# Kernel optimization log

Hardware: AMD Instinct MI355X
Metric: run time of the kernel (lower is better)

The kernel has to match this reference:

```python
import jax, jax.numpy as jnp
import numpy as np

NUM_CLASSES = 5  # config['training']['num_classes_per_task']


def _conv(x, w, b):
    # x: [N,C,H,W], w: [O,I,kh,kw] (torch OIHW), valid padding, stride 1
    y = jax.lax.conv_general_dilated(
        x, w, window_strides=(1, 1), padding='VALID',
        dimension_numbers=('NCHW', 'OIHW', 'NCHW'))
    return y + b[None, :, None, None]


def _maxpool2(x):
    return jax.lax.reduce_window(x, -jnp.inf, jax.lax.max,
                                 (1, 1, 2, 2), (1, 1, 2, 2), 'VALID')


def _lenet(x, c1w, c1b, c2w, c2b, f1w, f1b, f2w, f2b, f3w, f3b):
    h = _maxpool2(jax.nn.relu(_conv(x, c1w, c1b)))   # [N,6,14,14]
    h = _maxpool2(jax.nn.relu(_conv(h, c2w, c2b)))   # [N,16,5,5]
    h = h.reshape(h.shape[0], -1)                     # [N,400]
    h = jax.nn.relu(h @ f1w.T + f1b)                  # [N,120]
    h = jax.nn.relu(h @ f2w.T + f2b)                  # [N,84]
    return h @ f3w.T + f3b                            # [N,64] embeddings


def setup_inputs() -> dict:
    key = jax.random.key(0)
    ks = jax.random.split(key, 7)
    def w(k, shape, fan_in):
        return jax.random.normal(k, shape, jnp.float32) * (1.0 / np.sqrt(fan_in))
    return {
        'x': jax.random.normal(ks[0], (20480, 3, 32, 32), jnp.float32),
        'c1w': w(ks[1], (6, 3, 5, 5), 3 * 25), 'c1b': jnp.zeros((6,), jnp.float32),
        'c2w': w(ks[2], (16, 6, 5, 5), 6 * 25), 'c2b': jnp.zeros((16,), jnp.float32),
        'f1w': w(ks[3], (120, 400), 400), 'f1b': jnp.zeros((120,), jnp.float32),
        'f2w': w(ks[4], (84, 120), 120), 'f2b': jnp.zeros((84,), jnp.float32),
        'f3w': w(ks[5], (64, 84), 84), 'f3b': jnp.zeros((64,), jnp.float32),
    }


def reference(x, c1w, c1b, c2w, c2b, f1w, f1b, f2w, f2b, f3w, f3b):
    emb = _lenet(x, c1w, c1b, c2w, c2b, f1w, f1b, f2w, f2b, f3w, f3b)  # [N,64]
    # prototypes = embeddings.sum() / num_classes  (scalar, as in source)
    proto = emb.sum() / NUM_CLASSES
    result = jax.nn.softmax(emb, axis=1)
    # sqrt((result - proto)^2) elementwise == |result - proto|; the python
    # per-sample list-comprehension just rebuilds this same [N,64] tensor.
    return jnp.sqrt(jnp.square(result - proto))
```

## Files before the change

### kernel.cpp

```cpp
#include <hip/hip_runtime.h>
#include <math.h>

typedef __attribute__((ext_vector_type(8))) short short8;
typedef __attribute__((ext_vector_type(4))) float f32x4;
typedef __attribute__((ext_vector_type(4))) unsigned short us4v;

__device__ __forceinline__ unsigned short f2bf(float f) {
    unsigned u = __float_as_uint(f);
    return (unsigned short)((u + 0x7FFFu + ((u >> 16) & 1u)) >> 16);
}
__device__ __forceinline__ unsigned cvtpk(float lo, float hi) {
    unsigned r;
    asm("v_cvt_pk_bf16_f32 %0, %1, %2" : "=v"(r) : "v"(lo), "v"(hi));
    return r;
}
__device__ __forceinline__ unsigned short f2bf1(float v) {
    return (unsigned short)(cvtpk(v, 0.f) & 0xffffu);
}
__device__ __forceinline__ float fmax_x8(float v) {
    int s = __builtin_amdgcn_mov_dpp(__float_as_int(v), 0x128, 0xf, 0xf, true);
    return fmaxf(v, __int_as_float(s));
}

#define C1T_SS 3464
#define C1_RS 36
#define P1R 1176
#define P2S 424
#define A1S 136
#define A2S 104

__global__ __launch_bounds__(256, 3) void conv12fc_mfma(
    const float* __restrict__ x,
    const unsigned short* __restrict__ c1wf, const float* __restrict__ c1b,
    const unsigned short* __restrict__ c2wf, const float* __restrict__ c2b,
    const unsigned short* __restrict__ wb1, const float* __restrict__ f1b,
    const unsigned short* __restrict__ wb2, const float* __restrict__ f2b,
    const unsigned short* __restrict__ wb3, const float* __restrict__ f3b,
    float* __restrict__ emb, float* __restrict__ part)
{
    __shared__ __align__(16) unsigned short img[2 * C1T_SS];
    __shared__ __align__(16) unsigned short p1s[16 * P1R + 16];
    __shared__ float rsum[4];
    const int t = threadIdx.x;
    const int lane = t & 63, w = t >> 6;
    const int grp = lane >> 4, c = lane & 15;
    const int smp = c >> 3, q = c & 7;

    if (t < 192) {
        int s = t / 96, rr = t - s * 96;
        *(uint2*)&img[s * C1T_SS + rr * C1_RS + 32] = make_uint2(0u, 0u);
    }
    if (t < 2) {
        *(uint4*)&img[t * C1T_SS + 3456] = make_uint4(0u, 0u, 0u, 0u);
        *(uint4*)&p1s[16 * P1R + t * 8] = make_uint4(0u, 0u, 0u, 0u);
    }

    short8 wf1[5][4];
#pragma unroll
    for (int s = 0; s < 5; s++)
#pragma unroll
        for (int off = 0; off < 4; off++)
            wf1[s][off] = *(const short8*)&c1wf[(((s * 4 + off) * 4 + grp) * 16 + c) * 8];
    int ciA[5], kpA[5];
#pragma unroll
    for (int s = 0; s < 5; s++) {
        int b = s * 4 + grp; if (b > 17) b = 17;
        ciA[s] = b / 6; kpA[s] = b % 6;
    }
    const float bias1 = (c < 6) ? c1b[c] : 0.f;

    const float4* xs4 = (const float4*)(x + (size_t)blockIdx.x * 49152);
    float4 r[6];

#pragma unroll
    for (int k = 0; k < 6; k++) r[k] = xs4[k * 256 + t];

    for (int st = 0; st < 8; st++) {
#pragma unroll
        for (int k = 0; k < 6; k++) {
            int f = k * 256 + t;
            int s = (f >= 768) ? 1 : 0;
            int w4 = f - s * 768;
            int ci = w4 >> 8, rem = w4 & 255, y = rem >> 3, xq = rem & 7;
            uint2 pk = make_uint2(cvtpk(r[k].x, r[k].y), cvtpk(r[k].z, r[k].w));
            *(uint2*)&img[s * C1T_SS + (ci * 32 + y) * C1_RS + xq * 4] = pk;
        }
        __syncthreads();

        if (st < 7) {
#pragma unroll
            for (int k = 0; k < 6; k++) r[k] = xs4[(st + 1) * 1536 + k * 256 + t];
        }

        for (int py = w; py < 14; py += 4) {
            f32x4 a00 = {0.f,0.f,0.f,0.f}, a01 = a00, a10 = a00, a11 = a00;
#pragma unroll
            for (int s = 0; s < 5; s++) {
                int e = smp * C1T_SS + (ciA[s] * 32 + py * 2 + kpA[s]) * C1_RS + q * 4;
                union { us4v h[2]; short8 v; } af;
                af.h[0] = *(const us4v*)&img[e];
                af.h[1] = *(const us4v*)&img[e + 4];
                a00 = __builtin_amdgcn_mfma_f32_16x16x32_bf16(af.v, wf1[s][0], a00, 0, 0, 0);
                a01 = __builtin_amdgcn_mfma_f32_16x16x32_bf16(af.v, wf1[s][1], a01, 0, 0, 0);
                a10 = __builtin_amdgcn_mfma_f32_16x16x32_bf16(af.v, wf1[s][2], a10, 0, 0, 0);
                a11 = __builtin_amdgcn_mfma_f32_16x16x32_bf16(af.v, wf1[s][3], a11, 0, 0, 0);
            }
            f32x4 pe2, po2;
#pragma unroll
            for (int i = 0; i < 4; i++) {
                pe2[i] = fmax_x8(fmaxf(a00[i], a01[i]));
                po2[i] = fmax_x8(fmaxf(a10[i], a11[i]));
            }
            if (c < 6) {
#pragma unroll
                for (int i = 0; i < 4; i++) {
                    int m = grp * 4 + i;
                    int qo = m & 7;
                    if (qo < 7) {
                        int sm = m >> 3;
                        float v0 = fmaxf(pe2[i] + bias1, 0.f);
                        float v1 = fmaxf(po2[i] + bias1, 0.f);
                        *(unsigned*)&p1s[(2 * st + sm) * P1R + (c * 14 + py) * 14 + qo * 2]
                            = cvtpk(v0, v1);
                    }
                }
            }
        }
        __syncthreads();
    }

    short8 wf2[8][2];
#pragma unroll
    for (int s = 0; s < 8; s++)
#pragma unroll
        for (int off = 0; off < 2; off++)
            wf2[s][off] = *(const short8*)&c2wf[(((s * 2 + off) * 4 + grp) * 16 + c) * 8];
    int ciB[8], kyB[8];
#pragma unroll
    for (int s = 0; s < 8; s++) {
        int b = s * 4 + grp; if (b > 29) b = 29;
        ciB[s] = b / 5; kyB[s] = b % 5;
    }
    const float bias2 = c2b[c];

    unsigned pkbuf[7][2];
#pragma unroll
    for (int j = 0; j < 7; j++) {
        const int item = w + j * 4;
        if (item < 25) {
            const int py = item / 5, px = item % 5;
            f32x4 a00 = {0.f,0.f,0.f,0.f}, a01 = a00, a10 = a00, a11 = a00;
#pragma unroll
            for (int s = 0; s < 8; s++) {
                int rbase = ciB[s] * 14 + kyB[s] + py * 2;
#pragma unroll
                for (int yo = 0; yo < 2; yo++) {
                    int e = c * P1R + (rbase + yo) * 14 + px * 2;
                    union { unsigned u[4]; short8 v; } af;
                    af.u[0] = *(const unsigned*)&p1s[e];
                    af.u[1] = *(const unsigned*)&p1s[e + 2];
                    af.u[2] = *(const unsigned*)&p1s[e + 4];
                    af.u[3] = *(const unsigned*)&p1s[e + 6];
                    if (yo == 0) {
                        a00 = __builtin_amdgcn_mfma_f32_16x16x32_bf16(af.v, wf2[s][0], a00, 0, 0, 0);
                        a01 = __builtin_amdgcn_mfma_f32_16x16x32_bf16(af.v, wf2[s][1], a01, 0, 0, 0);
                    } else {
                        a10 = __builtin_amdgcn_mfma_f32_16x16x32_bf16(af.v, wf2[s][0], a10, 0, 0, 0);
                        a11 = __builtin_amdgcn_mfma_f32_16x16x32_bf16(af.v, wf2[s][1], a11, 0, 0, 0);
                    }
                }
            }
            float v0 = fmaxf(fmaxf(fmaxf(a00[0], a01[0]), fmaxf(a10[0], a11[0])) + bias2, 0.f);
            float v1 = fmaxf(fmaxf(fmaxf(a00[1], a01[1]), fmaxf(a10[1], a11[1])) + bias2, 0.f);
            float v2 = fmaxf(fmaxf(fmaxf(a00[2], a01[2]), fmaxf(a10[2], a11[2])) + bias2, 0.f);
            float v3 = fmaxf(fmaxf(fmaxf(a00[3], a01[3]), fmaxf(a10[3], a11[3])) + bias2, 0.f);
            pkbuf[j][0] = cvtpk(v0, v1);
            pkbuf[j][1] = cvtpk(v2, v3);
        }
    }
    __syncthreads();

    unsigned short* p2t = p1s;
#pragma unroll
    for (int j = 0; j < 7; j++) {
        const int item = w + j * 4;
        if (item < 25) {
#pragma unroll
            for (int i = 0; i < 4; i++) {
                unsigned v = pkbuf[j][i >> 1] >> ((i & 1) * 16);
                p2t[(grp * 4 + i) * P2S + c * 25 + item] = (unsigned short)v;
            }
        }
    }
    if (t < 32) {
        int s = t >> 1, h = t & 1;
        *(uint4*)&p2t[s * P2S + 400 + h * 8] = make_uint4(0u, 0u, 0u, 0u);
    }
    __syncthreads();

    unsigned short* a1s = img;
    unsigned short* a2s = img + 16 * A1S;
    {
        f32x4 acc[2] = {{0.f,0.f,0.f,0.f},{0.f,0.f,0.f,0.f}};
        const int sb = c * P2S;
#pragma unroll
        for (int ks = 0; ks < 13; ks++) {
            short8 a = *(const short8*)&p2t[sb + ks * 32 + grp * 8];
#pragma unroll
            for (int j = 0; j < 2; j++) {
                int o = (w + 4 * j) * 16 + c;
                short8 b = *(const short8*)&wb1[o * 416 + ks * 32 + grp * 8];
                acc[j] = __builtin_amdgcn_mfma_f32_16x16x32_bf16(a, b, acc[j], 0, 0, 0);
            }
        }
        __syncthreads();
#pragma unroll
        for (int j = 0; j < 2; j++) {
            int o = (w + 4 * j) * 16 + c;
            float bias = (o < 120) ? f1b[o] : 0.f;
#pragma unroll
            for (int i = 0; i < 4; i++)
                a1s[(grp * 4 + i) * A1S + o] = f2bf1(fmaxf(acc[j][i] + bias, 0.f));
        }
    }
    __syncthreads();

    {
        f32x4 acc[2] = {{0.f,0.f,0.f,0.f},{0.f,0.f,0.f,0.f}};
        const int sb = c * A1S;
#pragma unroll
        for (int ks = 0; ks < 4; ks++) {
            short8 a = *(const short8*)&a1s[sb + ks * 32 + grp * 8];
#pragma unroll
            for (int j = 0; j < 2; j++) {
                int nt = w + 4 * j;
                if (nt < 6) {
                    int o = nt * 16 + c;
                    short8 b = *(const short8*)&wb2[o * 128 + ks * 32 + grp * 8];
                    acc[j] = __builtin_amdgcn_mfma_f32_16x16x32_bf16(a, b, acc[j], 0, 0, 0);
                }
            }
        }
        __syncthreads();
#pragma unroll
        for (int j = 0; j < 2; j++) {
            int nt = w + 4 * j;
            if (nt < 6) {
                int o = nt * 16 + c;
                float bias = (o < 84) ? f2b[o] : 0.f;
#pragma unroll
                for (int i = 0; i < 4; i++)
                    a2s[(grp * 4 + i) * A2S + o] = f2bf1(fmaxf(acc[j][i] + bias, 0.f));
            }
        }
    }
    __syncthreads();

    {
        f32x4 acc = {0.f,0.f,0.f,0.f};
        const int sb = c * A2S;
        const int o = w * 16 + c;
#pragma unroll
        for (int ks = 0; ks < 3; ks++) {
            short8 a = *(const short8*)&a2s[sb + ks * 32 + grp * 8];
            short8 b = *(const short8*)&wb3[o * 96 + ks * 32 + grp * 8];
            acc = __builtin_amdgcn_mfma_f32_16x16x32_bf16(a, b, acc, 0, 0, 0);
        }
        const float bias = f3b[o];
        float psum = 0.f;
#pragma unroll
        for (int i = 0; i < 4; i++) {
            float v = acc[i] + bias;
            emb[((size_t)blockIdx.x * 16 + grp * 4 + i) * 64 + o] = v;
            psum += v;
        }
#pragma unroll
        for (int off = 32; off; off >>= 1) psum += __shfl_xor(psum, off);
        if (lane == 0) rsum[w] = psum;
        __syncthreads();
        if (t == 0) part[blockIdx.x] = (rsum[0] + rsum[1]) + (rsum[2] + rsum[3]);
    }
}

__global__ __launch_bounds__(256) void prep_weights(
    const float* __restrict__ c1w, const float* __restrict__ c2w,
    const float* __restrict__ f1w, const float* __restrict__ f2w,
    const float* __restrict__ f3w,
    unsigned short* __restrict__ wb1, unsigned short* __restrict__ wb2,
    unsigned short* __restrict__ wb3,
    unsigned short* __restrict__ c1wf, unsigned short* __restrict__ c2wf)
{
    const int t0 = blockIdx.x * 256 + threadIdx.x;
    const int stride = gridDim.x * 256;
    for (int i = t0; i < 128 * 416; i += stride) {
        int o = i / 416, k = i % 416;
        wb1[i] = f2bf((o < 120 && k < 400) ? f1w[o * 400 + k] : 0.f);
    }
    for (int i = t0; i < 96 * 128; i += stride) {
        int o = i / 128, k = i % 128;
        wb2[i] = f2bf((o < 84 && k < 120) ? f2w[o * 120 + k] : 0.f);
    }
    for (int i = t0; i < 64 * 96; i += stride) {
        int o = i / 96, k = i % 96;
        wb3[i] = f2bf((k < 84) ? f3w[o * 84 + k] : 0.f);
    }
    for (int i = t0; i < 10240; i += stride) {
        int j = i & 7, c = (i >> 3) & 15, grp = (i >> 7) & 3;
        int off = (i >> 9) & 3, s = i >> 11;
        int b = s * 4 + grp;
        int ci = b / 6, kp = b % 6;
        int kx = j - off;
        float v = 0.f;
        if (b < 18 && kx >= 0 && kx <= 4) {
            if (c < 6 && kp <= 4)
                v = c1w[c * 75 + ci * 25 + kp * 5 + kx];
            else if (c >= 8 && c < 14 && kp >= 1)
                v = c1w[(c - 8) * 75 + ci * 25 + (kp - 1) * 5 + kx];
        }
        c1wf[i] = f2bf(v);
    }
    for (int i = t0; i < 8192; i += stride) {
        int j = i & 7, c = (i >> 3) & 15, grp = (i >> 7) & 3;
        int off = (i >> 9) & 1, s = i >> 10;
        int b = s * 4 + grp;
        int kx = j - off;
        float v = 0.f;
        if (b < 30 && kx >= 0 && kx <= 4) {
            int ci = b / 5, ky = b % 5;
            v = c2w[c * 150 + ci * 25 + ky * 5 + kx];
        }
        c2wf[i] = f2bf(v);
    }
}

__global__ __launch_bounds__(256) void softmax_abs(float* __restrict__ io,
                                                   const float* __restrict__ part) {
    const int lane = threadIdx.x & 63;
    const int row = (blockIdx.x << 2) + (threadIdx.x >> 6);
    float e = io[(size_t)row * 64 + lane];
    float ps = 0.f;
#pragma unroll
    for (int k = 0; k < 20; k++) ps += part[k * 64 + lane];
#pragma unroll
    for (int off = 32; off; off >>= 1) ps += __shfl_xor(ps, off);
    const float proto = ps / 5.0f;
    float m = e;
#pragma unroll
    for (int off = 32; off; off >>= 1) m = fmaxf(m, __shfl_xor(m, off));
    float p = expf(e - m);
    float s = p;
#pragma unroll
    for (int off = 32; off; off >>= 1) s += __shfl_xor(s, off);
    io[(size_t)row * 64 + lane] = fabsf(p / s - proto);
}

extern "C" void kernel_launch(void* const* d_in, const int* in_sizes, int n_in,
                              void* d_out, int out_size, void* d_ws, size_t ws_size,
                              hipStream_t stream) {
    const float* x   = (const float*)d_in[0];
    const float* c1w = (const float*)d_in[1];
    const float* c1b = (const float*)d_in[2];
    const float* c2w = (const float*)d_in[3];
    const float* c2b = (const float*)d_in[4];
    const float* f1w = (const float*)d_in[5];
    const float* f1b = (const float*)d_in[6];
    const float* f2w = (const float*)d_in[7];
    const float* f2b = (const float*)d_in[8];
    const float* f3w = (const float*)d_in[9];
    const float* f3b = (const float*)d_in[10];
    float* out = (float*)d_out;

    const int N = in_sizes[0] / 3072;
    float* part = (float*)d_ws;
    unsigned short* wb1  = (unsigned short*)((char*)d_ws + 8192);
    unsigned short* wb2  = wb1 + 128 * 416;
    unsigned short* wb3  = wb2 + 96 * 128;
    unsigned short* c1wf = wb3 + 64 * 96;
    unsigned short* c2wf = c1wf + 10240;

    prep_weights<<<64, 256, 0, stream>>>(c1w, c2w, f1w, f2w, f3w,
                                         wb1, wb2, wb3, c1wf, c2wf);
    conv12fc_mfma<<<N / 16, 256, 0, stream>>>(x, c1wf, c1b, c2wf, c2b,
                                              wb1, f1b, wb2, f2b, wb3, f3b,
                                              out, part);
    softmax_abs<<<N / 4, 256, 0, stream>>>(out, part);
}
```

Before: 94.26 us.

## Halve samples per block and reuse shifted conv1 fragments to cut registers and LDS

Each block now handles 8 samples instead of 16, which halves the pooled-conv1 LDS buffer and doubles the grid. Occupancy is raised to 4 blocks per CU. Conv1 keeps only two weight fragments and builds the odd-x input fragment by shifting loaded bf16 values, so register use drops. Conv2 maps the y-offset into lanes instead of separate accumulators. The FC stages now mask off half of their MFMA rows, which wastes MFMA work, and the softmax kernel reads twice as many partial sums.

```diff
diff --git a/kernel.cpp b/kernel.cpp
--- a/kernel.cpp
+++ b/kernel.cpp
@@ -29,7 +29,7 @@
 #define A1S 136
 #define A2S 104
 
-__global__ __launch_bounds__(256, 3) void conv12fc_mfma(
+__global__ __launch_bounds__(256, 4) void conv12fc_mfma(
     const float* __restrict__ x,
     const unsigned short* __restrict__ c1wf, const float* __restrict__ c1b,
     const unsigned short* __restrict__ c2wf, const float* __restrict__ c2b,
@@ -39,7 +39,7 @@
     float* __restrict__ emb, float* __restrict__ part)
 {
     __shared__ __align__(16) unsigned short img[2 * C1T_SS];
-    __shared__ __align__(16) unsigned short p1s[16 * P1R + 16];
+    __shared__ __align__(16) unsigned short p1s[8 * P1R + 16];
     __shared__ float rsum[4];
     const int t = threadIdx.x;
     const int lane = t & 63, w = t >> 6;
@@ -52,14 +52,14 @@
     }
     if (t < 2) {
         *(uint4*)&img[t * C1T_SS + 3456] = make_uint4(0u, 0u, 0u, 0u);
-        *(uint4*)&p1s[16 * P1R + t * 8] = make_uint4(0u, 0u, 0u, 0u);
-    }
-
-    short8 wf1[5][4];
+        *(uint4*)&p1s[8 * P1R + t * 8] = make_uint4(0u, 0u, 0u, 0u);
+    }
+
+    short8 wf1[5][2];
 #pragma unroll
     for (int s = 0; s < 5; s++)
 #pragma unroll
-        for (int off = 0; off < 4; off++)
+        for (int off = 0; off < 2; off++)
             wf1[s][off] = *(const short8*)&c1wf[(((s * 4 + off) * 4 + grp) * 16 + c) * 8];
     int ciA[5], kpA[5];
 #pragma unroll
@@ -69,13 +69,13 @@
     }
     const float bias1 = (c < 6) ? c1b[c] : 0.f;
 
-    const float4* xs4 = (const float4*)(x + (size_t)blockIdx.x * 49152);
+    const float4* xs4 = (const float4*)(x + (size_t)blockIdx.x * 24576);
     float4 r[6];
 
 #pragma unroll
     for (int k = 0; k < 6; k++) r[k] = xs4[k * 256 + t];
 
-    for (int st = 0; st < 8; st++) {
+    for (int st = 0; st < 4; st++) {
 #pragma unroll
         for (int k = 0; k < 6; k++) {
             int f = k * 256 + t;
@@ -87,7 +87,7 @@
         }
         __syncthreads();
 
-        if (st < 7) {
+        if (st < 3) {
 #pragma unroll
             for (int k = 0; k < 6; k++) r[k] = xs4[(st + 1) * 1536 + k * 256 + t];
         }
@@ -97,13 +97,17 @@
 #pragma unroll
             for (int s = 0; s < 5; s++) {
                 int e = smp * C1T_SS + (ciA[s] * 32 + py * 2 + kpA[s]) * C1_RS + q * 4;
-                union { us4v h[2]; short8 v; } af;
-                af.h[0] = *(const us4v*)&img[e];
-                af.h[1] = *(const us4v*)&img[e + 4];
-                a00 = __builtin_amdgcn_mfma_f32_16x16x32_bf16(af.v, wf1[s][0], a00, 0, 0, 0);
-                a01 = __builtin_amdgcn_mfma_f32_16x16x32_bf16(af.v, wf1[s][1], a01, 0, 0, 0);
-                a10 = __builtin_amdgcn_mfma_f32_16x16x32_bf16(af.v, wf1[s][2], a10, 0, 0, 0);
-                a11 = __builtin_amdgcn_mfma_f32_16x16x32_bf16(af.v, wf1[s][3], a11, 0, 0, 0);
+                us4v h0 = *(const us4v*)&img[e];
+                us4v h1 = *(const us4v*)&img[e + 4];
+                ushort2 h2 = *(const ushort2*)&img[e + 8];
+                short8 A0 = { (short)h0[0],(short)h0[1],(short)h0[2],(short)h0[3],
+                              (short)h1[0],(short)h1[1],(short)h1[2],(short)h1[3] };
+                short8 A2 = { (short)h0[2],(short)h0[3],(short)h1[0],(short)h1[1],
+                              (short)h1[2],(short)h1[3],(short)h2.x,(short)h2.y };
+                a00 = __builtin_amdgcn_mfma_f32_16x16x32_bf16(A0, wf1[s][0], a00, 0, 0, 0);
+                a01 = __builtin_amdgcn_mfma_f32_16x16x32_bf16(A0, wf1[s][1], a01, 0, 0, 0);
+                a10 = __builtin_amdgcn_mfma_f32_16x16x32_bf16(A2, wf1[s][0], a10, 0, 0, 0);
+                a11 = __builtin_amdgcn_mfma_f32_16x16x32_bf16(A2, wf1[s][1], a11, 0, 0, 0);
             }
             f32x4 pe2, po2;
 #pragma unroll
@@ -142,40 +146,30 @@
         ciB[s] = b / 5; kyB[s] = b % 5;
     }
     const float bias2 = c2b[c];
-
-    unsigned pkbuf[7][2];
+    const int arow2 = (c >> 1) * P1R;
+    const int yoff = c & 1;
+
+    unsigned pkbuf[7];
 #pragma unroll
     for (int j = 0; j < 7; j++) {
         const int item = w + j * 4;
         if (item < 25) {
             const int py = item / 5, px = item % 5;
-            f32x4 a00 = {0.f,0.f,0.f,0.f}, a01 = a00, a10 = a00, a11 = a00;
+            f32x4 a0 = {0.f,0.f,0.f,0.f}, a1 = a0;
 #pragma unroll
             for (int s = 0; s < 8; s++) {
-                int rbase = ciB[s] * 14 + kyB[s] + py * 2;
-#pragma unroll
-                for (int yo = 0; yo < 2; yo++) {
-                    int e = c * P1R + (rbase + yo) * 14 + px * 2;
-                    union { unsigned u[4]; short8 v; } af;
-                    af.u[0] = *(const unsigned*)&p1s[e];
-                    af.u[1] = *(const unsigned*)&p1s[e + 2];
-                    af.u[2] = *(const unsigned*)&p1s[e + 4];
-                    af.u[3] = *(const unsigned*)&p1s[e + 6];
-                    if (yo == 0) {
-                        a00 = __builtin_amdgcn_mfma_f32_16x16x32_bf16(af.v, wf2[s][0], a00, 0, 0, 0);
-                        a01 = __builtin_amdgcn_mfma_f32_16x16x32_bf16(af.v, wf2[s][1], a01, 0, 0, 0);
-                    } else {
-                        a10 = __builtin_amdgcn_mfma_f32_16x16x32_bf16(af.v, wf2[s][0], a10, 0, 0, 0);
-                        a11 = __builtin_amdgcn_mfma_f32_16x16x32_bf16(af.v, wf2[s][1], a11, 0, 0, 0);
-                    }
-                }
-            }
-            float v0 = fmaxf(fmaxf(fmaxf(a00[0], a01[0]), fmaxf(a10[0], a11[0])) + bias2, 0.f);
-            float v1 = fmaxf(fmaxf(fmaxf(a00[1], a01[1]), fmaxf(a10[1], a11[1])) + bias2, 0.f);
-            float v2 = fmaxf(fmaxf(fmaxf(a00[2], a01[2]), fmaxf(a10[2], a11[2])) + bias2, 0.f);
-            float v3 = fmaxf(fmaxf(fmaxf(a00[3], a01[3]), fmaxf(a10[3], a11[3])) + bias2, 0.f);
-            pkbuf[j][0] = cvtpk(v0, v1);
-            pkbuf[j][1] = cvtpk(v2, v3);
+                int e = arow2 + (ciB[s] * 14 + py * 2 + yoff + kyB[s]) * 14 + px * 2;
+                union { unsigned u[4]; short8 v; } af;
+                af.u[0] = *(const unsigned*)&p1s[e];
+                af.u[1] = *(const unsigned*)&p1s[e + 2];
+                af.u[2] = *(const unsigned*)&p1s[e + 4];
+                af.u[3] = *(const unsigned*)&p1s[e + 6];
+                a0 = __builtin_amdgcn_mfma_f32_16x16x32_bf16(af.v, wf2[s][0], a0, 0, 0, 0);
+                a1 = __builtin_amdgcn_mfma_f32_16x16x32_bf16(af.v, wf2[s][1], a1, 0, 0, 0);
+            }
+            float v0 = fmaxf(fmaxf(fmaxf(a0[0], a0[1]), fmaxf(a1[0], a1[1])) + bias2, 0.f);
+            float v1 = fmaxf(fmaxf(fmaxf(a0[2], a0[3]), fmaxf(a1[2], a1[3])) + bias2, 0.f);
+            pkbuf[j] = cvtpk(v0, v1);
         }
     }
     __syncthreads();
@@ -185,11 +179,8 @@
     for (int j = 0; j < 7; j++) {
         const int item = w + j * 4;
         if (item < 25) {
-#pragma unroll
-            for (int i = 0; i < 4; i++) {
-                unsigned v = pkbuf[j][i >> 1] >> ((i & 1) * 16);
-                p2t[(grp * 4 + i) * P2S + c * 25 + item] = (unsigned short)v;
-            }
+            p2t[(grp * 2 + 0) * P2S + c * 25 + item] = (unsigned short)(pkbuf[j] & 0xffffu);
+            p2t[(grp * 2 + 1) * P2S + c * 25 + item] = (unsigned short)(pkbuf[j] >> 16);
         }
     }
     if (t < 32) {
@@ -219,8 +210,10 @@
             int o = (w + 4 * j) * 16 + c;
             float bias = (o < 120) ? f1b[o] : 0.f;
 #pragma unroll
-            for (int i = 0; i < 4; i++)
-                a1s[(grp * 4 + i) * A1S + o] = f2bf1(fmaxf(acc[j][i] + bias, 0.f));
+            for (int i = 0; i < 4; i++) {
+                int s = grp * 4 + i;
+                if (s < 8) a1s[s * A1S + o] = f2bf1(fmaxf(acc[j][i] + bias, 0.f));
+            }
         }
     }
     __syncthreads();
@@ -249,8 +242,10 @@
                 int o = nt * 16 + c;
                 float bias = (o < 84) ? f2b[o] : 0.f;
 #pragma unroll
-                for (int i = 0; i < 4; i++)
-                    a2s[(grp * 4 + i) * A2S + o] = f2bf1(fmaxf(acc[j][i] + bias, 0.f));
+                for (int i = 0; i < 4; i++) {
+                    int s = grp * 4 + i;
+                    if (s < 8) a2s[s * A2S + o] = f2bf1(fmaxf(acc[j][i] + bias, 0.f));
+                }
             }
         }
     }
@@ -270,9 +265,12 @@
         float psum = 0.f;
 #pragma unroll
         for (int i = 0; i < 4; i++) {
-            float v = acc[i] + bias;
-            emb[((size_t)blockIdx.x * 16 + grp * 4 + i) * 64 + o] = v;
-            psum += v;
+            int s = grp * 4 + i;
+            if (s < 8) {
+                float v = acc[i] + bias;
+                emb[((size_t)blockIdx.x * 8 + s) * 64 + o] = v;
+                psum += v;
+            }
         }
 #pragma unroll
         for (int off = 32; off; off >>= 1) psum += __shfl_xor(psum, off);
@@ -340,7 +338,7 @@
     float e = io[(size_t)row * 64 + lane];
     float ps = 0.f;
 #pragma unroll
-    for (int k = 0; k < 20; k++) ps += part[k * 64 + lane];
+    for (int k = 0; k < 40; k++) ps += part[k * 64 + lane];
 #pragma unroll
     for (int off = 32; off; off >>= 1) ps += __shfl_xor(ps, off);
     const float proto = ps / 5.0f;
@@ -372,7 +370,7 @@
 
     const int N = in_sizes[0] / 3072;
     float* part = (float*)d_ws;
-    unsigned short* wb1  = (unsigned short*)((char*)d_ws + 8192);
+    unsigned short* wb1  = (unsigned short*)((char*)d_ws + 16384);
     unsigned short* wb2  = wb1 + 128 * 416;
     unsigned short* wb3  = wb2 + 96 * 128;
     unsigned short* c1wf = wb3 + 64 * 96;
@@ -380,8 +378,8 @@
 
     prep_weights<<<64, 256, 0, stream>>>(c1w, c2w, f1w, f2w, f3w,
                                          wb1, wb2, wb3, c1wf, c2wf);
-    conv12fc_mfma<<<N / 16, 256, 0, stream>>>(x, c1wf, c1b, c2wf, c2b,
-                                              wb1, f1b, wb2, f2b, wb3, f3b,
-                                              out, part);
+    conv12fc_mfma<<<N / 8, 256, 0, stream>>>(x, c1wf, c1b, c2wf, c2b,
+                                             wb1, f1b, wb2, f2b, wb3, f3b,
+                                             out, part);
     softmax_abs<<<N / 4, 256, 0, stream>>>(out, part);
 }
```

Measured after the change: 106.6 us. +13.1%, slower.
